# Kernel optimization log

Hardware: AMD Instinct MI355X
Metric: run time of the kernel (lower is better)

The kernel has to match this reference:

```python
import jax, jax.numpy as jnp
import numpy as np

NUM_ENTITIES = 600
FIRST_ENTITY = 0
LAST_ENTITY = 511  # inclusive, as in attentions[:, first:last+1]
EPS = 1e-9


def setup_inputs() -> dict:
    key = jax.random.key(0)
    k1, k2, k3, k4 = jax.random.split(key, 4)
    B, S, E = 64, 4096, 128
    doc_emb = jax.random.normal(k1, (B, S, E), dtype=jnp.float32)
    query_emb = jax.random.normal(k2, (B, E), dtype=jnp.float32)
    doc_ids = jax.random.randint(k3, (B, S), 0, NUM_ENTITIES, dtype=jnp.int32)
    seq_length = jax.random.randint(k4, (B,), 0, S, dtype=jnp.int32)
    return {"doc_emb": doc_emb, "query_emb": query_emb,
            "doc_ids": doc_ids, "seq_length": seq_length}


def reference(doc_emb, query_emb, doc_ids, seq_length):
    B, S, E = doc_emb.shape
    # --- _calculate_attention: batched mat-vec + length-masked softmax ---
    scores = jnp.einsum('bse,be->bs', doc_emb, query_emb)          # [B,S]
    seq_len = jnp.maximum(seq_length, 1)                            # guard empty docs
    valid = jnp.arange(S)[None, :] < seq_len[:, None]               # [B,S] bool
    scores = jnp.where(valid, scores, jnp.float32(-1e30))
    attentions = jax.nn.softmax(scores, axis=-1)                    # [B,S]
    # --- _sum_attentions: per-batch unsorted_segment_sum over entity ids ---
    # offset trick replaces tf.map_fn-serialized segment sums with one batched scatter
    seg_ids = (doc_ids + jnp.arange(B, dtype=doc_ids.dtype)[:, None] * NUM_ENTITIES).reshape(-1)
    sums = jax.ops.segment_sum(attentions.reshape(-1), seg_ids,
                               num_segments=B * NUM_ENTITIES)
    sums = sums.reshape(B, NUM_ENTITIES)[:, FIRST_ENTITY:LAST_ENTITY + 1]  # [B,512]
    # --- softmax_inverse: log (eps for numerical safety on zero-mass entities) ---
    logits = jnp.log(sums + EPS)
    return logits
```

## Files before the change

### kernel.cpp

```cpp
#include <hip/hip_runtime.h>
#include <hip/hip_bf16.h>
#include <math.h>

#define BB 64
#define SS 4096
#define EE 128
#define NENT 600
#define NOUT 512

__global__ __launch_bounds__(256) void fused_kernel(
    const float* __restrict__ doc_emb,
    const float* __restrict__ query_emb,
    const int* __restrict__ doc_ids,
    const int* __restrict__ seq_length,
    float* __restrict__ bins,
    float* __restrict__ denom) {
  const int b     = blockIdx.y;
  const int chunk = blockIdx.x;
  const int tid   = threadIdx.x;
  const int wave  = tid >> 6;
  const int lane  = tid & 63;
  const int half  = lane >> 5;
  const int sub   = lane & 31;

  int len = seq_length[b];
  if (len < 1) len = 1;

  const float4 q = ((const float4*)(query_emb + b * EE))[sub];
  const float* base = doc_emb + (size_t)b * SS * EE;
  const int* ids = doc_ids + b * SS;
  float* mybins = bins + b * NENT;

  const int s0 = chunk * 128 + wave * 2 + half;
  float dsum = 0.f;

#pragma unroll
  for (int it = 0; it < 16; ++it) {
    const int s = s0 + it * 8;
    const float4 d = ((const float4*)(base + (size_t)s * EE))[sub];
    float p = d.x * q.x + d.y * q.y + d.z * q.z + d.w * q.w;
#pragma unroll
    for (int off = 16; off; off >>= 1) p += __shfl_down(p, off, 32);
    if (sub == 0 && s < len) {
      const float e = __expf(p);
      atomicAdd(&mybins[ids[s]], e);
      dsum += e;
    }
  }
  dsum += __shfl_down(dsum, 32, 64);
  if (lane == 0 && dsum > 0.f) atomicAdd(&denom[b], dsum);
}

__global__ __launch_bounds__(512) void finalize_kernel(
    const float* __restrict__ bins,
    const float* __restrict__ denom,
    float* __restrict__ out) {
  const int b = blockIdx.x;
  const float inv = 1.f / denom[b];
  const int e = threadIdx.x;
  out[b * NOUT + e] = logf(bins[b * NENT + e] * inv + 1e-9f);
}

extern "C" void kernel_launch(void* const* d_in, const int* in_sizes, int n_in,
                              void* d_out, int out_size, void* d_ws, size_t ws_size,
                              hipStream_t stream) {
  const float* doc_emb    = (const float*)d_in[0];
  const float* query_emb  = (const float*)d_in[1];
  const int*   doc_ids    = (const int*)d_in[2];
  const int*   seq_length = (const int*)d_in[3];
  float* out   = (float*)d_out;
  float* bins  = (float*)d_ws;
  float* denom = bins + BB * NENT;

  hipMemsetAsync(d_ws, 0, (size_t)(BB * NENT + BB) * sizeof(float), stream);

  fused_kernel<<<dim3(SS / 128, BB), 256, 0, stream>>>(
      doc_emb, query_emb, doc_ids, seq_length, bins, denom);
  finalize_kernel<<<BB, NOUT, 0, stream>>>(bins, denom, out);
}
```

Measured before the change: 221.1 us.

## Bin attentions in shared memory per chunk and merge partials without memset

New measurement: 192.1 us. 13.1% less time.

```diff
diff --git a/kernel.cpp b/kernel.cpp
--- a/kernel.cpp
+++ b/kernel.cpp
@@ -7,14 +7,18 @@
 #define EE 128
 #define NENT 600
 #define NOUT 512
+#define NCHUNK 32
+#define ROWS_PER_BLOCK 128
 
-__global__ __launch_bounds__(256) void fused_kernel(
+typedef float v4f __attribute__((ext_vector_type(4)));
+
+__global__ __launch_bounds__(256) void fused_bin_kernel(
     const float* __restrict__ doc_emb,
     const float* __restrict__ query_emb,
     const int* __restrict__ doc_ids,
     const int* __restrict__ seq_length,
-    float* __restrict__ bins,
-    float* __restrict__ denom) {
+    float* __restrict__ pbins,
+    float* __restrict__ pdenom) {
   const int b     = blockIdx.y;
   const int chunk = blockIdx.x;
   const int tid   = threadIdx.x;
@@ -23,42 +27,72 @@
   const int half  = lane >> 5;
   const int sub   = lane & 31;
 
+  __shared__ float lbins[NOUT];
+  __shared__ float wden[4];
+
+  lbins[tid]       = 0.f;
+  lbins[tid + 256] = 0.f;
+  __syncthreads();
+
   int len = seq_length[b];
   if (len < 1) len = 1;
 
-  const float4 q = ((const float4*)(query_emb + b * EE))[sub];
+  const v4f q = ((const v4f*)(query_emb + b * EE))[sub];
   const float* base = doc_emb + (size_t)b * SS * EE;
   const int* ids = doc_ids + b * SS;
-  float* mybins = bins + b * NENT;
 
-  const int s0 = chunk * 128 + wave * 2 + half;
+  const int s0 = chunk * ROWS_PER_BLOCK + wave * 2 + half;
   float dsum = 0.f;
 
 #pragma unroll
   for (int it = 0; it < 16; ++it) {
     const int s = s0 + it * 8;
-    const float4 d = ((const float4*)(base + (size_t)s * EE))[sub];
+    const v4f d =
+        __builtin_nontemporal_load(((const v4f*)(base + (size_t)s * EE)) + sub);
     float p = d.x * q.x + d.y * q.y + d.z * q.z + d.w * q.w;
 #pragma unroll
     for (int off = 16; off; off >>= 1) p += __shfl_down(p, off, 32);
     if (sub == 0 && s < len) {
       const float e = __expf(p);
-      atomicAdd(&mybins[ids[s]], e);
       dsum += e;
+      const int id = ids[s];
+      if (id < NOUT) atomicAdd(&lbins[id], e);
     }
   }
+
   dsum += __shfl_down(dsum, 32, 64);
-  if (lane == 0 && dsum > 0.f) atomicAdd(&denom[b], dsum);
+  if (lane == 0) wden[wave] = dsum;
+  __syncthreads();
+
+  float* ob = pbins + (size_t)(b * NCHUNK + chunk) * NOUT;
+  ob[tid]       = lbins[tid];
+  ob[tid + 256] = lbins[tid + 256];
+  if (tid == 0)
+    pdenom[b * NCHUNK + chunk] = wden[0] + wden[1] + wden[2] + wden[3];
 }
 
-__global__ __launch_bounds__(512) void finalize_kernel(
-    const float* __restrict__ bins,
-    const float* __restrict__ denom,
+__global__ __launch_bounds__(512) void merge_kernel(
+    const float* __restrict__ pbins,
+    const float* __restrict__ pdenom,
     float* __restrict__ out) {
-  const int b = blockIdx.x;
-  const float inv = 1.f / denom[b];
-  const int e = threadIdx.x;
-  out[b * NOUT + e] = logf(bins[b * NENT + e] * inv + 1e-9f);
+  const int b   = blockIdx.x;
+  const int tid = threadIdx.x;
+  __shared__ float s_inv;
+
+  if (tid < NCHUNK) {
+    float d = pdenom[b * NCHUNK + tid];
+#pragma unroll
+    for (int off = 16; off; off >>= 1) d += __shfl_down(d, off, 32);
+    if (tid == 0) s_inv = 1.f / d;
+  }
+
+  float s = 0.f;
+  const float* pb = pbins + (size_t)b * NCHUNK * NOUT + tid;
+#pragma unroll
+  for (int c = 0; c < NCHUNK; ++c) s += pb[c * NOUT];
+  __syncthreads();
+
+  out[b * NOUT + tid] = logf(s * s_inv + 1e-9f);
 }
 
 extern "C" void kernel_launch(void* const* d_in, const int* in_sizes, int n_in,
@@ -68,13 +102,11 @@
   const float* query_emb  = (const float*)d_in[1];
   const int*   doc_ids    = (const int*)d_in[2];
   const int*   seq_length = (const int*)d_in[3];
-  float* out   = (float*)d_out;
-  float* bins  = (float*)d_ws;
-  float* denom = bins + BB * NENT;
+  float* out    = (float*)d_out;
+  float* pbins  = (float*)d_ws;
+  float* pdenom = pbins + BB * NCHUNK * NOUT;
 
-  hipMemsetAsync(d_ws, 0, (size_t)(BB * NENT + BB) * sizeof(float), stream);
-
-  fused_kernel<<<dim3(SS / 128, BB), 256, 0, stream>>>(
-      doc_emb, query_emb, doc_ids, seq_length, bins, denom);
-  finalize_kernel<<<BB, NOUT, 0, stream>>>(bins, denom, out);
+  fused_bin_kernel<<<dim3(NCHUNK, BB), 256, 0, stream>>>(
+      doc_emb, query_emb, doc_ids, seq_length, pbins, pdenom);
+  merge_kernel<<<BB, NOUT, 0, stream>>>(pbins, pdenom, out);
 }
```
